# Kernel tuning notes

Measured on AMD Instinct MI355X. Metric: run time of the kernel, lower is better.

The kernel has to match this reference:

```python
import jax, jax.numpy as jnp
import numpy as np

B, S, N = 4, 512, 2048
E = 1024          # expanded_size
QL, H, D, VL = 32, 8, 2, 32   # query_len, num_heads, num_duplicates, values_len
EPS = 1e-5


def setup_inputs() -> dict:
    key = jax.random.key(0)
    ks = jax.random.split(key, 8)
    return {
        "embeddings": jax.random.normal(ks[0], (B, S, E), jnp.float32),
        "keys": jax.random.normal(ks[1], (B, N, QL * H), jnp.float32),
        "values": jax.random.normal(ks[2], (B, N, VL * H), jnp.float32),
        "output_connectivity_sub": jax.random.normal(ks[3], (H, S * D, N), jnp.float32),
        "Wq": jax.random.normal(ks[4], (QL * H * D, E), jnp.float32) / np.sqrt(E),
        "bq": jnp.zeros((QL * H * D,), jnp.float32),
        "Wo": jax.random.normal(ks[5], (E, VL * H * D), jnp.float32) / np.sqrt(VL * H * D),
        "bo": jnp.zeros((E,), jnp.float32),
        "gamma": jnp.ones((VL * H * D,), jnp.float32),
        "beta": jnp.zeros((VL * H * D,), jnp.float32),
    }


def reference(embeddings, keys, values, output_connectivity_sub,
              Wq, bq, Wo, bo, gamma, beta):
    # query projection: [B,S,E] -> [B,S,QL*H*D]
    q = embeddings @ Wq.T + bq
    # view [B, S*D, QL*H] -> [B, S*D, QL, H] -> [B, H, S*D, QL]
    q = q.reshape(B, S * D, QL, H).transpose(0, 3, 1, 2)
    # keys: [B,N,QL*H] -> [B,N,QL,H] -> [B,H,QL,N]
    k = keys.reshape(B, N, QL, H).transpose(0, 3, 2, 1)
    # values: [B,N,VL*H] -> [B,N,VL,H] -> [B,H,N,VL]
    v = values.reshape(B, N, VL, H).transpose(0, 3, 1, 2)

    scores = jnp.einsum('bhsq,bhqn->bhsn', q, k) / np.sqrt(QL).astype(np.float32)
    probs = jax.nn.softmax(scores - output_connectivity_sub, axis=-1)
    vo = jnp.einsum('bhsn,bhnv->bhsv', probs, v)          # [B,H,S*D,VL]

    # [B,H,S*D,VL] -> [B,H,S,VL*D] -> [B,S,H,VL*D] -> [B,S,H*VL*D]
    vo = vo.reshape(B, H, S, VL * D).transpose(0, 2, 1, 3).reshape(B, S, H * VL * D)

    mean = jnp.mean(vo, axis=-1, keepdims=True)
    var = jnp.mean(jnp.square(vo - mean), axis=-1, keepdims=True)
    xn = (vo - mean) / jnp.sqrt(var + EPS) * gamma + beta
    return xn @ Wo.T + bo
```

## Files before the change

kernel.cpp:

```cpp
#include <hip/hip_runtime.h>
#include <hip/hip_bf16.h>


typedef short  short8 __attribute__((ext_vector_type(8)));
typedef float  f32x4  __attribute__((ext_vector_type(4)));

__device__ __forceinline__ ushort f2bf(float x) {
  union { float f; unsigned int u; } v; v.f = x;
  unsigned int r = v.u + 0x7fffu + ((v.u >> 16) & 1u);
  return (ushort)(r >> 16);
}

__device__ __forceinline__ unsigned int cvtpk(float a, float b) {
  unsigned int r;
  asm("v_cvt_pk_bf16_f32 %0, %1, %2" : "=v"(r) : "v"(a), "v"(b));
  return r;
}
__device__ __forceinline__ short8 cvt8(f32x4 a, f32x4 b) {
  union { unsigned int u[4]; short8 s; } r;
  r.u[0] = cvtpk(a[0], a[1]);
  r.u[1] = cvtpk(a[2], a[3]);
  r.u[2] = cvtpk(b[0], b[1]);
  r.u[3] = cvtpk(b[2], b[3]);
  return r.s;
}

#if __has_builtin(__builtin_amdgcn_global_load_lds)
#define OCS_ASYNC 1
__device__ __forceinline__ void gl_lds16(const float* g, float* l) {
  __builtin_amdgcn_global_load_lds(
      (const __attribute__((address_space(1))) unsigned int*)g,
      (__attribute__((address_space(3))) unsigned int*)l, 16, 0, 0);
}
#else
#define OCS_ASYNC 0
#endif

__global__ __launch_bounds__(256) void prep_kv(
    const float* __restrict__ keys, const float* __restrict__ values,
    ushort* __restrict__ kbf, ushort* __restrict__ vbf)
{
  __shared__ ushort T[32][264];
  const int bi = blockIdx.x;
  const int b  = bi >> 6;
  const int n0 = (bi & 63) * 32;
  const int t  = threadIdx.x;
  const int nr = t >> 3;
  const int c0 = (t & 7) * 32;

  {
    const float* src = keys + ((size_t)b*2048 + n0 + nr)*256 + c0;
#pragma unroll
    for (int j = 0; j < 32; j += 8) {
      f32x4 x0 = *(const f32x4*)(src + j);
      f32x4 x1 = *(const f32x4*)(src + j + 4);
      *(short8*)&T[nr][c0 + j] = cvt8(x0, x1);
    }
  }
  __syncthreads();
  {
    const int h = t >> 5, nn = t & 31;
    const int pp = 16*((nn >> 2) & 1) + 4*(nn >> 3) + (nn & 3);
    ushort* dst = kbf + (((size_t)(b*8 + h) * 2048) + n0 + pp) * 32;
#pragma unroll
    for (int j = 0; j < 4; j++) {
      short8 w;
#pragma unroll
      for (int i = 0; i < 8; i++) w[i] = (short)T[nn][(j*8 + i)*8 + h];
      *(short8*)(dst + j*8) = w;
    }
  }
  __syncthreads();
  {
    const float* src = values + ((size_t)b*2048 + n0 + nr)*256 + c0;
#pragma unroll
    for (int j = 0; j < 32; j += 8) {
      f32x4 x0 = *(const f32x4*)(src + j);
      f32x4 x1 = *(const f32x4*)(src + j + 4);
      *(short8*)&T[nr][c0 + j] = cvt8(x0, x1);
    }
  }
  __syncthreads();
  {
    const int c = t, h = c & 7, vl = c >> 3;
    ushort* dst = vbf + (((size_t)(b*8 + h) * 32) + vl) * 2048 + n0;
#pragma unroll
    for (int j = 0; j < 4; j++) {
      short8 w;
#pragma unroll
      for (int i = 0; i < 8; i++) w[i] = (short)T[j*8 + i][c];
      *(short8*)(dst + j*8) = w;
    }
  }
}

template<int EPI>
__global__ __launch_bounds__(256) void gemm_nt(
    const float* __restrict__ A, const float* __restrict__ Bm,
    const float* __restrict__ bias, void* __restrict__ outp,
    int M, int N, int K)
{
  __shared__ ushort As[2][64][32];
  __shared__ ushort Bs[2][64][32];
  const int tid = threadIdx.x;
  const int m0 = blockIdx.x * 64;
  const int n0 = blockIdx.y * 64;
  const int lane = tid & 63;
  const int wid  = tid >> 6;
  const int wm = wid >> 1, wn = wid & 1;
  const int lt = lane & 15, g = lane >> 4;
  const int lrow = tid >> 2;
  const int lseg = tid & 3;
  const int slot_w = lseg ^ ((lrow & 3) ^ ((lrow >> 2) & 3));
  const int sa_r = (g ^ ((( wm*32 + lt) & 3) ^ (((wm*32 + lt) >> 2) & 3)));

  f32x4 acc[2][2] = {};
  f32x4 pa0, pa1, pb0, pb1;

#define GLOAD(K0) do {                                                        \
    const float* sa_ = A  + (size_t)(m0 + lrow) * K + (K0) + lseg * 8;        \
    pa0 = *(const f32x4*)sa_;  pa1 = *(const f32x4*)(sa_ + 4);                \
    const float* sb_ = Bm + (size_t)(n0 + lrow) * K + (K0) + lseg * 8;        \
    pb0 = *(const f32x4*)sb_;  pb1 = *(const f32x4*)(sb_ + 4);                \
  } while (0)
#define SWRITE(BUF) do {                                                      \
    *(short8*)&As[BUF][lrow][slot_w * 8] = cvt8(pa0, pa1);                    \
    *(short8*)&Bs[BUF][lrow][slot_w * 8] = cvt8(pb0, pb1);                    \
  } while (0)

  GLOAD(0);
  SWRITE(0);
  __syncthreads();

  int cur = 0;
  for (int k0 = 0; k0 < K; k0 += 32) {
    const bool more = (k0 + 32 < K);
    if (more) GLOAD(k0 + 32);
    short8 af[2], bfr[2];
#pragma unroll
    for (int ss = 0; ss < 2; ss++) {
      const int ra = wm*32 + ss*16 + lt;
      af[ss]  = *(const short8*)&As[cur][ra][(g ^ ((ra & 3) ^ ((ra >> 2) & 3))) * 8];
      const int rb = wn*32 + ss*16 + lt;
      bfr[ss] = *(const short8*)&Bs[cur][rb][(g ^ ((rb & 3) ^ ((rb >> 2) & 3))) * 8];
    }
#pragma unroll
    for (int i = 0; i < 2; i++)
#pragma unroll
      for (int j = 0; j < 2; j++)
        acc[i][j] = __builtin_amdgcn_mfma_f32_16x16x32_bf16(af[i], bfr[j], acc[i][j], 0, 0, 0);
    asm volatile("s_barrier" ::: "memory");
    if (more) {
      SWRITE(cur ^ 1);
      asm volatile("s_waitcnt lgkmcnt(0)" ::: "memory");
    }
    asm volatile("s_barrier" ::: "memory");
    cur ^= 1;
  }

#pragma unroll
  for (int i = 0; i < 2; i++)
#pragma unroll
    for (int j = 0; j < 2; j++) {
      const int n  = n0 + wn*32 + j*16 + lt;
      const float bv = bias[n];
      const int mb = m0 + wm*32 + i*16 + g*4;
#pragma unroll
      for (int r = 0; r < 4; r++) {
        const int mm = mb + r;
        if (EPI == 0) {
          const float val = (acc[i][j][r] + bv) * 0.17677669529663687f;
          const int bb = mm >> 9, s = mm & 511;
          const int d = n >> 8, ql = (n >> 3) & 31, hh = n & 7;
          const int tt = s*2 + d;
          ((ushort*)outp)[((size_t)(bb*8 + hh) * 1024 + tt) * 32 + ql] = f2bf(val);
        } else {
          ((float*)outp)[(size_t)mm * N + n] = acc[i][j][r] + bv;
        }
      }
    }
#undef GLOAD
#undef SWRITE
}

__global__ __launch_bounds__(256) void attn_kernel(
    const ushort* __restrict__ qbf, const ushort* __restrict__ kbf,
    const ushort* __restrict__ vbf, const float* __restrict__ ocs,
    float* __restrict__ pacc, float* __restrict__ pl, int nsteps)
{
#if OCS_ASYNC
  __shared__ float obuf[4][2048];
#endif
  const int tid  = threadIdx.x;
  const int lane = tid & 63;
  const int id = blockIdx.x;
  const int h   = id & 7;
  const int ttp = (id >> 3) & 15;
  const int c   = id >> 7;
  const int b  = tid >> 6;
  const int wid0 = ((h << 5) + 2*ttp) * 4 + b;
  const int t0 = ttp * 64;
  const int lt = lane & 15, g = lane >> 4;
  const int n_start = c * nsteps * 32;

  const ushort* qp = qbf + (size_t)(b*8 + h) * (1024*32);
  const ushort* kp = kbf + (size_t)(b*8 + h) * (2048*32);
  const ushort* vp = vbf + (size_t)(b*8 + h) * (32*2048);
  const float*  op = ocs + (size_t)h * (1024*2048);

#define NSX(I) (((I) < nsteps) ? (n_start + (I)*32) : n_start)

  const int srow = tid >> 3;
  const int scol = 4 * ((tid & 7) ^ (srow & 7));
  const float* sb0 = op + (size_t)(t0 + srow) * 2048 + scol;
  const float* sb1 = op + (size_t)(t0 + 32 + srow) * 2048 + scol;
#if OCS_ASYNC
  const int ldsw = (tid & 192) * 16;
#define SL_ISSUE(STEP) do {                                                   \
    gl_lds16(sb0 + NSX(STEP), (float*)((char*)obuf + (((STEP) & 3) << 13) + ldsw));        \
    gl_lds16(sb1 + NSX(STEP), (float*)((char*)obuf + (((STEP) & 3) << 13) + 4096 + ldsw)); \
  } while (0)
  const int ro0 = lt * 128;
  const int ro1 = (16 + lt) * 128;
  const int c0x = ((2*g)     ^ (lt & 7)) * 16;
  const int c1x = ((2*g + 1) ^ (lt & 7)) * 16;
#define CO_READ(DST, TILE, STEP) do {                                         \
    const char* bb_ = (const char*)obuf + (((STEP) & 3) << 13) + ((TILE) << 12); \
    DST[0][0] = *(const f32x4*)(bb_ + ro0 + c0x);                             \
    DST[1][0] = *(const f32x4*)(bb_ + ro0 + c1x);                             \
    DST[0][1] = *(const f32x4*)(bb_ + ro1 + c0x);                             \
    DST[1][1] = *(const f32x4*)(bb_ + ro1 + c1x);                             \
  } while (0)
#define PAIR_SYNC() do {                                                      \
    __builtin_amdgcn_sched_barrier(0);                                        \
    asm volatile("s_waitcnt vmcnt(8)" ::: "memory");                          \
    __builtin_amdgcn_sched_barrier(0);                                        \
    __builtin_amdgcn_s_barrier();                                             \
  } while (0)
#else
#define SL_ISSUE(STEP)
#define CO_READ(DST, TILE, STEP) do {                                         \
    const int nn_ = NSX(STEP);                                                \
    const float* r0_ = op + (size_t)(t0 + (TILE)*32 + lt) * 2048 + nn_;       \
    const float* r1_ = op + (size_t)(t0 + (TILE)*32 + 16 + lt) * 2048 + nn_;  \
    DST[0][0] = *(const f32x4*)(r0_ + 8*g);                                   \
    DST[1][0] = *(const f32x4*)(r0_ + 8*g + 4);                               \
    DST[0][1] = *(const f32x4*)(r1_ + 8*g);                                   \
    DST[1][1] = *(const f32x4*)(r1_ + 8*g + 4);                               \
  } while (0)
#define PAIR_SYNC()
#endif

#define LD_KV(KD, VD, NN) do {                                                \
    KD[0] = *(const short8*)(kp + (size_t)((NN) + lt) * 32 + g*8);            \
    KD[1] = *(const short8*)(kp + (size_t)((NN) + 16 + lt) * 32 + g*8);       \
    VD[0] = *(const short8*)(vp + (size_t)lt * 2048 + (NN) + g*8);            \
    VD[1] = *(const short8*)(vp + (size_t)(16 + lt) * 2048 + (NN) + g*8);     \
  } while (0)

  short8 qf0[2], qf1[2];
#pragma unroll
  for (int ts = 0; ts < 2; ts++) {
    qf0[ts] = *(const short8*)(qp + (t0 + ts*16 + lt)*32 + g*8);
    qf1[ts] = *(const short8*)(qp + (t0 + 32 + ts*16 + lt)*32 + g*8);
  }

  f32x4 acc0[2][2] = {}, acc1[2][2] = {};
  float lsum0[2] = {0.f, 0.f}, lsum1[2] = {0.f, 0.f};
  const f32x4 fzero = {0.f, 0.f, 0.f, 0.f};

#define TSB(SC0, SC1, CO0, CO1, VLO, VHI, LS, ACCA, ACCB) do {                \
    float p0 = __expf(SC0[0] - CO0[0]);                                       \
    float p1 = __expf(SC0[1] - CO0[1]);                                       \
    float p2 = __expf(SC0[2] - CO0[2]);                                       \
    float p3 = __expf(SC0[3] - CO0[3]);                                       \
    float p4 = __expf(SC1[0] - CO1[0]);                                       \
    float p5 = __expf(SC1[1] - CO1[1]);                                       \
    float p6 = __expf(SC1[2] - CO1[2]);                                       \
    float p7 = __expf(SC1[3] - CO1[3]);                                       \
    LS += ((p0+p1)+(p2+p3)) + ((p4+p5)+(p6+p7));                              \
    union { unsigned int u[4]; short8 s; } pf;                                \
    pf.u[0] = (unsigned int)f2bf(p0) | ((unsigned int)f2bf(p1) << 16);        \
    pf.u[1] = (unsigned int)f2bf(p2) | ((unsigned int)f2bf(p3) << 16);        \
    pf.u[2] = (unsigned int)f2bf(p4) | ((unsigned int)f2bf(p5) << 16);        \
    pf.u[3] = (unsigned int)f2bf(p6) | ((unsigned int)f2bf(p7) << 16);        \
    ACCA = __builtin_amdgcn_mfma_f32_16x16x32_bf16(VLO, pf.s, ACCA, 0, 0, 0); \
    ACCB = __builtin_amdgcn_mfma_f32_16x16x32_bf16(VHI, pf.s, ACCB, 0, 0, 0); \
  } while (0)

#define STEPTILE(KC_, VC_, QFA, QFB, TILE, STEP, ACC, LS) do {                \
    f32x4 s0a = __builtin_amdgcn_mfma_f32_16x16x32_bf16(KC_[0], QFA, fzero, 0, 0, 0); \
    f32x4 s1a = __builtin_amdgcn_mfma_f32_16x16x32_bf16(KC_[1], QFA, fzero, 0, 0, 0); \
    f32x4 s0b = __builtin_amdgcn_mfma_f32_16x16x32_bf16(KC_[0], QFB, fzero, 0, 0, 0); \
    f32x4 s1b = __builtin_amdgcn_mfma_f32_16x16x32_bf16(KC_[1], QFB, fzero, 0, 0, 0); \
    f32x4 co[2][2];                                                           \
    CO_READ(co, TILE, STEP);                                                  \
    TSB(s0a, s1a, co[0][0], co[1][0], VC_[0], VC_[1], LS[0], ACC[0][0], ACC[0][1]); \
    TSB(s0b, s1b, co[0][1], co[1][1], VC_[0], VC_[1], LS[1], ACC[1][0], ACC[1][1]); \
  } while (0)

#define PAIR(SA_, KC, VC, KN, VN) do {                                        \
    const int sA_ = (SA_);                                                    \
    SL_ISSUE(sA_ + 2);                                                        \
    SL_ISSUE(sA_ + 3);                                                        \
    __builtin_amdgcn_sched_barrier(0);                                        \
    LD_KV(KN[0], VN[0], NSX(sA_ + 2));                                        \
    LD_KV(KN[1], VN[1], NSX(sA_ + 3));                                        \
    __builtin_amdgcn_sched_barrier(0);                                        \
    STEPTILE(KC[0], VC[0], qf0[0], qf0[1], 0, sA_,     acc0, lsum0);          \
    STEPTILE(KC[0], VC[0], qf1[0], qf1[1], 1, sA_,     acc1, lsum1);          \
    STEPTILE(KC[1], VC[1], qf0[0], qf0[1], 0, sA_ + 1, acc0, lsum0);          \
    STEPTILE(KC[1], VC[1], qf1[0], qf1[1], 1, sA_ + 1, acc1, lsum1);          \
    PAIR_SYNC();                                                              \
  } while (0)

  short8 KA[2][2], VA[2][2], KB[2][2], VB[2][2];

#if OCS_ASYNC
  SL_ISSUE(0); SL_ISSUE(1);
  __builtin_amdgcn_sched_barrier(0);
#endif
  LD_KV(KA[0], VA[0], NSX(0));
  LD_KV(KA[1], VA[1], NSX(1));
#if OCS_ASYNC
  __builtin_amdgcn_sched_barrier(0);
  asm volatile("s_waitcnt vmcnt(8)" ::: "memory");
  __builtin_amdgcn_s_barrier();
#endif

  for (int s = 0; s < nsteps; s += 4) {
    PAIR(s,     KA, VA, KB, VB);
    PAIR(s + 2, KB, VB, KA, VA);
  }
#undef PAIR
#undef STEPTILE
#undef TSB
#undef LD_KV
#undef CO_READ
#undef SL_ISSUE
#undef PAIR_SYNC
#undef NSX

  {
    float* pb0 = pacc + ((size_t)(c*1024 + wid0) * 4) * 256 + lane * 4;
    *(f32x4*)(pb0 + 0*256) = acc0[0][0];
    *(f32x4*)(pb0 + 1*256) = acc0[0][1];
    *(f32x4*)(pb0 + 2*256) = acc0[1][0];
    *(f32x4*)(pb0 + 3*256) = acc0[1][1];
    float* pb1 = pacc + ((size_t)(c*1024 + wid0 + 4) * 4) * 256 + lane * 4;
    *(f32x4*)(pb1 + 0*256) = acc1[0][0];
    *(f32x4*)(pb1 + 1*256) = acc1[0][1];
    *(f32x4*)(pb1 + 2*256) = acc1[1][0];
    *(f32x4*)(pb1 + 3*256) = acc1[1][1];
  }
#pragma unroll
  for (int ts = 0; ts < 2; ts++) {
    float L0 = lsum0[ts], L1 = lsum1[ts];
    L0 += __shfl_xor(L0, 16);  L0 += __shfl_xor(L0, 32);
    L1 += __shfl_xor(L1, 16);  L1 += __shfl_xor(L1, 32);
    if (g == 0) {
      pl[((size_t)(c*1024 + wid0)) * 32 + ts*16 + lt]     = L0;
      pl[((size_t)(c*1024 + wid0 + 4)) * 32 + ts*16 + lt] = L1;
    }
  }
}

__global__ __launch_bounds__(256) void combine_kernel(
    const float* __restrict__ pacc, const float* __restrict__ pl,
    float* __restrict__ vo, int NS)
{
  const int lane = threadIdx.x & 63;
  const int wid = blockIdx.x * 4 + (threadIdx.x >> 6);
  const int b  = wid & 3;
  const int tt = (wid >> 2) & 31;
  const int h  = wid >> 7;
  const int t0 = tt * 32;
  const int lt = lane & 15, g = lane >> 4;

  f32x4 acc[4] = {};
  float L[2] = {0.f, 0.f};
  for (int cc = 0; cc < NS; ++cc) {
    const float* pb = pacc + ((size_t)(cc*1024 + wid) * 4) * 256 + lane * 4;
#pragma unroll
    for (int q = 0; q < 4; q++) {
      f32x4 v = *(const f32x4*)(pb + q * 256);
#pragma unroll
      for (int r = 0; r < 4; r++) acc[q][r] += v[r];
    }
    L[0] += pl[((size_t)(cc*1024 + wid)) * 32 + lt];
    L[1] += pl[((size_t)(cc*1024 + wid)) * 32 + 16 + lt];
  }
#pragma unroll
  for (int ts = 0; ts < 2; ts++) {
    const float inv = 1.0f / L[ts];
    const int t = t0 + ts*16 + lt;
    const int s = t >> 1, d = t & 1;
    float* dst = vo + ((size_t)(b*512 + s) * 512) + h*64 + d*32;
#pragma unroll
    for (int vs = 0; vs < 2; vs++) {
      f32x4 o;
#pragma unroll
      for (int r = 0; r < 4; r++) o[r] = acc[ts*2 + vs][r] * inv;
      *(f32x4*)(dst + vs*16 + g*4) = o;
    }
  }
}

__global__ __launch_bounds__(256) void ln_kernel(
    const float* __restrict__ x_in, const float* __restrict__ gamma,
    const float* __restrict__ beta, float* __restrict__ x_out)
{
  const int row  = blockIdx.x * 4 + (threadIdx.x >> 6);
  const int lane = threadIdx.x & 63;
  const float* x = x_in + (size_t)row * 512 + lane * 8;
  f32x4 v0 = *(const f32x4*)x;
  f32x4 v1 = *(const f32x4*)(x + 4);
  float s = (v0[0]+v0[1]+v0[2]+v0[3]) + (v1[0]+v1[1]+v1[2]+v1[3]);
#pragma unroll
  for (int off = 1; off < 64; off <<= 1) s += __shfl_xor(s, off);
  const float mean = s * (1.0f/512.0f);
  float var = 0.f;
#pragma unroll
  for (int i = 0; i < 4; i++) {
    float d0 = v0[i]-mean, d1 = v1[i]-mean;
    var += d0*d0 + d1*d1;
  }
#pragma unroll
  for (int off = 1; off < 64; off <<= 1) var += __shfl_xor(var, off);
  const float rstd = rsqrtf(var * (1.0f/512.0f) + 1e-5f);
  const float* gp = gamma + lane*8;
  const float* bp = beta  + lane*8;
  f32x4 g0 = *(const f32x4*)gp, g1 = *(const f32x4*)(gp+4);
  f32x4 b0 = *(const f32x4*)bp, b1 = *(const f32x4*)(bp+4);
  f32x4 o0, o1;
#pragma unroll
  for (int i = 0; i < 4; i++) {
    o0[i] = (v0[i]-mean)*rstd*g0[i] + b0[i];
    o1[i] = (v1[i]-mean)*rstd*g1[i] + b1[i];
  }
  float* o = x_out + (size_t)row * 512 + lane * 8;
  *(f32x4*)o = o0;
  *(f32x4*)(o + 4) = o1;
}

extern "C" void kernel_launch(void* const* d_in, const int* in_sizes, int n_in,
                              void* d_out, int out_size, void* d_ws, size_t ws_size,
                              hipStream_t stream)
{
  const float* emb    = (const float*)d_in[0];
  const float* keys   = (const float*)d_in[1];
  const float* values = (const float*)d_in[2];
  const float* ocs    = (const float*)d_in[3];
  const float* Wq     = (const float*)d_in[4];
  const float* bq     = (const float*)d_in[5];
  const float* Wo     = (const float*)d_in[6];
  const float* bo     = (const float*)d_in[7];
  const float* gamma  = (const float*)d_in[8];
  const float* beta   = (const float*)d_in[9];

  char* ws = (char*)d_ws;
  ushort* qbf = (ushort*)(ws);
  ushort* kbf = (ushort*)(ws + (2u << 20));
  ushort* vbf = (ushort*)(ws + (6u << 20));
  float*  vo  = (float*) (ws + (10u << 20));
  const size_t pbase = (size_t)14u << 20;

  int NS;
  if      (ws_size >= ((size_t)48u << 20)) NS = 8;
  else if (ws_size >= ((size_t)31u << 20)) NS = 4;
  else if (ws_size >= ((size_t)23u << 20)) NS = 2;
  else                                     NS = 1;
  float* pacc = (float*)(ws + pbase);
  float* pl   = (float*)(ws + pbase + (size_t)NS * (4u << 20));
  const int nsteps = 2048 / (NS * 32);

  prep_kv<<<dim3(256), dim3(256), 0, stream>>>(keys, values, kbf, vbf);
  gemm_nt<0><<<dim3(32, 8), dim3(256), 0, stream>>>(emb, Wq, bq, (void*)qbf, 2048, 512, 1024);
  attn_kernel<<<dim3(128 * NS), dim3(256), 0, stream>>>(qbf, kbf, vbf, ocs, pacc, pl, nsteps);
  combine_kernel<<<dim3(256), dim3(256), 0, stream>>>(pacc, pl, vo, NS);
  ln_kernel<<<dim3(512), dim3(256), 0, stream>>>(vo, gamma, beta, vo);
  gemm_nt<1><<<dim3(32, 16), dim3(256), 0, stream>>>(vo, Wo, bo, d_out, 2048, 1024, 512);
}
```

Baseline: 89.99 us.

## Merge prep and Q-projection launches; fold LayerNorm apply into output GEMM

Combines the K/V conversion kernel and the query-projection GEMM into one launch whose blocks branch by index, which removes a launch and lets the two independent jobs overlap. It also splits LayerNorm into a stats-only kernel that writes per-row mean and rstd. The output GEMM then applies normalization, gamma and beta while staging A tiles into LDS, which saves writing and re-reading the normalized activations. In exchange, each output GEMM tile reloads gamma/beta and recomputes the normalization, and the merged kernel shares one LDS size across both roles, which may lower occupancy for the prep blocks.

```diff
diff --git a/kernel.cpp b/kernel.cpp
--- a/kernel.cpp
+++ b/kernel.cpp
@@ -36,12 +36,12 @@
 #define OCS_ASYNC 0
 #endif
 
-__global__ __launch_bounds__(256) void prep_kv(
+__device__ __forceinline__ void prep_body(
+    char* smem, int bi,
     const float* __restrict__ keys, const float* __restrict__ values,
     ushort* __restrict__ kbf, ushort* __restrict__ vbf)
 {
-  __shared__ ushort T[32][264];
-  const int bi = blockIdx.x;
+  ushort (*T)[264] = (ushort (*)[264])smem;
   const int b  = bi >> 6;
   const int n0 = (bi & 63) * 32;
   const int t  = threadIdx.x;
@@ -95,16 +95,17 @@
 }
 
 template<int EPI>
-__global__ __launch_bounds__(256) void gemm_nt(
+__device__ __forceinline__ void gemm_body(
+    char* smem,
     const float* __restrict__ A, const float* __restrict__ Bm,
     const float* __restrict__ bias, void* __restrict__ outp,
-    int M, int N, int K)
-{
-  __shared__ ushort As[2][64][32];
-  __shared__ ushort Bs[2][64][32];
+    int M, int N, int K, int m0, int n0,
+    const float* __restrict__ lnmean, const float* __restrict__ lnrstd,
+    const float* __restrict__ gamma,  const float* __restrict__ beta)
+{
+  ushort* As = (ushort*)smem;
+  ushort* Bs = (ushort*)(smem + 8192);
   const int tid = threadIdx.x;
-  const int m0 = blockIdx.x * 64;
-  const int n0 = blockIdx.y * 64;
   const int lane = tid & 63;
   const int wid  = tid >> 6;
   const int wm = wid >> 1, wn = wid & 1;
@@ -112,10 +113,12 @@
   const int lrow = tid >> 2;
   const int lseg = tid & 3;
   const int slot_w = lseg ^ ((lrow & 3) ^ ((lrow >> 2) & 3));
-  const int sa_r = (g ^ ((( wm*32 + lt) & 3) ^ (((wm*32 + lt) >> 2) & 3)));
 
   f32x4 acc[2][2] = {};
   f32x4 pa0, pa1, pb0, pb1;
+
+  float mean_r = 0.f, rstd_r = 1.f;
+  if (EPI == 1) { mean_r = lnmean[m0 + lrow]; rstd_r = lnrstd[m0 + lrow]; }
 
 #define GLOAD(K0) do {                                                        \
     const float* sa_ = A  + (size_t)(m0 + lrow) * K + (K0) + lseg * 8;        \
@@ -123,13 +126,25 @@
     const float* sb_ = Bm + (size_t)(n0 + lrow) * K + (K0) + lseg * 8;        \
     pb0 = *(const f32x4*)sb_;  pb1 = *(const f32x4*)(sb_ + 4);                \
   } while (0)
-#define SWRITE(BUF) do {                                                      \
-    *(short8*)&As[BUF][lrow][slot_w * 8] = cvt8(pa0, pa1);                    \
-    *(short8*)&Bs[BUF][lrow][slot_w * 8] = cvt8(pb0, pb1);                    \
+#define SWRITE(BUF, K0) do {                                                  \
+    f32x4 qa0 = pa0, qa1 = pa1;                                               \
+    if (EPI == 1) {                                                           \
+      const float* gp_ = gamma + (K0) + lseg * 8;                             \
+      const float* bp_ = beta  + (K0) + lseg * 8;                             \
+      f32x4 g0_ = *(const f32x4*)gp_, g1_ = *(const f32x4*)(gp_ + 4);         \
+      f32x4 b0_ = *(const f32x4*)bp_, b1_ = *(const f32x4*)(bp_ + 4);         \
+      _Pragma("unroll")                                                       \
+      for (int r_ = 0; r_ < 4; r_++) {                                        \
+        qa0[r_] = (qa0[r_] - mean_r) * rstd_r * g0_[r_] + b0_[r_];            \
+        qa1[r_] = (qa1[r_] - mean_r) * rstd_r * g1_[r_] + b1_[r_];            \
+      }                                                                       \
+    }                                                                         \
+    *(short8*)&As[(BUF)*2048 + lrow*32 + slot_w * 8] = cvt8(qa0, qa1);        \
+    *(short8*)&Bs[(BUF)*2048 + lrow*32 + slot_w * 8] = cvt8(pb0, pb1);        \
   } while (0)
 
   GLOAD(0);
-  SWRITE(0);
+  SWRITE(0, 0);
   __syncthreads();
 
   int cur = 0;
@@ -140,9 +155,9 @@
 #pragma unroll
     for (int ss = 0; ss < 2; ss++) {
       const int ra = wm*32 + ss*16 + lt;
-      af[ss]  = *(const short8*)&As[cur][ra][(g ^ ((ra & 3) ^ ((ra >> 2) & 3))) * 8];
+      af[ss]  = *(const short8*)&As[cur*2048 + ra*32 + (g ^ ((ra & 3) ^ ((ra >> 2) & 3))) * 8];
       const int rb = wn*32 + ss*16 + lt;
-      bfr[ss] = *(const short8*)&Bs[cur][rb][(g ^ ((rb & 3) ^ ((rb >> 2) & 3))) * 8];
+      bfr[ss] = *(const short8*)&Bs[cur*2048 + rb*32 + (g ^ ((rb & 3) ^ ((rb >> 2) & 3))) * 8];
     }
 #pragma unroll
     for (int i = 0; i < 2; i++)
@@ -151,7 +166,7 @@
         acc[i][j] = __builtin_amdgcn_mfma_f32_16x16x32_bf16(af[i], bfr[j], acc[i][j], 0, 0, 0);
     asm volatile("s_barrier" ::: "memory");
     if (more) {
-      SWRITE(cur ^ 1);
+      SWRITE(cur ^ 1, k0 + 32);
       asm volatile("s_waitcnt lgkmcnt(0)" ::: "memory");
     }
     asm volatile("s_barrier" ::: "memory");
@@ -181,6 +196,36 @@
     }
 #undef GLOAD
 #undef SWRITE
+}
+
+__global__ __launch_bounds__(256) void prep_gemm0(
+    const float* __restrict__ keys, const float* __restrict__ values,
+    ushort* __restrict__ kbf, ushort* __restrict__ vbf,
+    const float* __restrict__ emb, const float* __restrict__ Wq,
+    const float* __restrict__ bq, ushort* __restrict__ qbf)
+{
+  __shared__ __align__(16) char smem[17408];
+  const int bi = blockIdx.x;
+  if (bi < 256) {
+    prep_body(smem, bi, keys, values, kbf, vbf);
+  } else {
+    const int gblk = bi - 256;
+    const int m0 = (gblk & 31) * 64;
+    const int n0 = (gblk >> 5) * 64;
+    gemm_body<0>(smem, emb, Wq, bq, (void*)qbf, 2048, 512, 1024, m0, n0,
+                 nullptr, nullptr, nullptr, nullptr);
+  }
+}
+
+__global__ __launch_bounds__(256) void gemm1_ln(
+    const float* __restrict__ vo, const float* __restrict__ Wo,
+    const float* __restrict__ bo, float* __restrict__ outp,
+    const float* __restrict__ lnmean, const float* __restrict__ lnrstd,
+    const float* __restrict__ gamma, const float* __restrict__ beta)
+{
+  __shared__ __align__(16) char smem[16384];
+  gemm_body<1>(smem, vo, Wo, bo, (void*)outp, 2048, 1024, 512,
+               blockIdx.x * 64, blockIdx.y * 64, lnmean, lnrstd, gamma, beta);
 }
 
 __global__ __launch_bounds__(256) void attn_kernel(
@@ -406,9 +451,9 @@
   }
 }
 
-__global__ __launch_bounds__(256) void ln_kernel(
-    const float* __restrict__ x_in, const float* __restrict__ gamma,
-    const float* __restrict__ beta, float* __restrict__ x_out)
+__global__ __launch_bounds__(256) void ln_stats(
+    const float* __restrict__ x_in, float* __restrict__ lnmean,
+    float* __restrict__ lnrstd)
 {
   const int row  = blockIdx.x * 4 + (threadIdx.x >> 6);
   const int lane = threadIdx.x & 63;
@@ -428,19 +473,10 @@
 #pragma unroll
   for (int off = 1; off < 64; off <<= 1) var += __shfl_xor(var, off);
   const float rstd = rsqrtf(var * (1.0f/512.0f) + 1e-5f);
-  const float* gp = gamma + lane*8;
-  const float* bp = beta  + lane*8;
-  f32x4 g0 = *(const f32x4*)gp, g1 = *(const f32x4*)(gp+4);
-  f32x4 b0 = *(const f32x4*)bp, b1 = *(const f32x4*)(bp+4);
-  f32x4 o0, o1;
-#pragma unroll
-  for (int i = 0; i < 4; i++) {
-    o0[i] = (v0[i]-mean)*rstd*g0[i] + b0[i];
-    o1[i] = (v1[i]-mean)*rstd*g1[i] + b1[i];
-  }
-  float* o = x_out + (size_t)row * 512 + lane * 8;
-  *(f32x4*)o = o0;
-  *(f32x4*)(o + 4) = o1;
+  if (lane == 0) {
+    lnmean[row] = mean;
+    lnrstd[row] = rstd;
+  }
 }
 
 extern "C" void kernel_launch(void* const* d_in, const int* in_sizes, int n_in,
@@ -472,12 +508,15 @@
   else                                     NS = 1;
   float* pacc = (float*)(ws + pbase);
   float* pl   = (float*)(ws + pbase + (size_t)NS * (4u << 20));
+  float* lnm  = (float*)(ws + pbase + (size_t)NS * (4u << 20) + (size_t)NS * (128u << 10));
+  float* lnr  = lnm + 2048;
   const int nsteps = 2048 / (NS * 32);
 
-  prep_kv<<<dim3(256), dim3(256), 0, stream>>>(keys, values, kbf, vbf);
-  gemm_nt<0><<<dim3(32, 8), dim3(256), 0, stream>>>(emb, Wq, bq, (void*)qbf, 2048, 512, 1024);
+  prep_gemm0<<<dim3(512), dim3(256), 0, stream>>>(keys, values, kbf, vbf,
+                                                  emb, Wq, bq, qbf);
   attn_kernel<<<dim3(128 * NS), dim3(256), 0, stream>>>(qbf, kbf, vbf, ocs, pacc, pl, nsteps);
   combine_kernel<<<dim3(256), dim3(256), 0, stream>>>(pacc, pl, vo, NS);
-  ln_kernel<<<dim3(512), dim3(256), 0, stream>>>(vo, gamma, beta, vo);
-  gemm_nt<1><<<dim3(32, 16), dim3(256), 0, stream>>>(vo, Wo, bo, d_out, 2048, 1024, 512);
-}
+  ln_stats<<<dim3(512), dim3(256), 0, stream>>>(vo, lnm, lnr);
+  gemm1_ln<<<dim3(32, 16), dim3(256), 0, stream>>>(vo, Wo, bo, (float*)d_out,
+                                                   lnm, lnr, gamma, beta);
+}
```

Result: faster. 86.49 us (-3.9%).
